# Optimization experiments

Measured on AMD Instinct MI355X. Metric: run time of the kernel, lower is better.

Reference implementation:

```python
import jax, jax.numpy as jnp
import numpy as np
import math

B, T, D, H = 4, 2048, 1024, 16
DH = D // H

def setup_inputs() -> dict:
    key = jax.random.key(0)
    k1, k2, k3, k4, k5 = jax.random.split(key, 5)
    s = 1.0 / math.sqrt(D)
    x = jax.random.normal(k1, (B, T, D), dtype=jnp.float32)
    # causal mask: 1 where attention allowed (j <= i), 0 elsewhere
    mask = jnp.tril(jnp.ones((T, T), dtype=jnp.float32))[None, None, :, :]
    W_qkv = jax.random.normal(k2, (D, 3 * D), dtype=jnp.float32) * s
    b_qkv = jax.random.normal(k3, (3 * D,), dtype=jnp.float32) * 0.02
    W_proj = jax.random.normal(k4, (D, D), dtype=jnp.float32) * s
    b_proj = jax.random.normal(k5, (D,), dtype=jnp.float32) * 0.02
    return {"x": x, "mask": mask, "W_qkv": W_qkv, "b_qkv": b_qkv,
            "W_proj": W_proj, "b_proj": b_proj}

def reference(x, mask, W_qkv, b_qkv, W_proj, b_proj):
    # qkv: [B,T,3D] -> [3,B,H,T,DH]
    qkv = x @ W_qkv + b_qkv
    qkv = qkv.reshape(B, T, 3, H, DH).transpose(2, 0, 3, 1, 4)
    q, k, v = qkv[0], qkv[1], qkv[2]
    scores = jnp.einsum('bhqd,bhkd->bhqk', q, k) / math.sqrt(DH)
    scores = jnp.where(mask == 0, -jnp.inf, scores)
    attn = jax.nn.softmax(scores, axis=-1)  # dropout p=0 -> identity
    out = jnp.einsum('bhqk,bhkd->bhqd', attn, v)
    out = out.transpose(0, 2, 1, 3).reshape(B, T, D)
    return out @ W_proj + b_proj
```

## Files before the change

kernel.cpp:

```cpp
#include <hip/hip_runtime.h>
#include <hip/hip_bf16.h>

typedef __attribute__((ext_vector_type(8))) short short8;
typedef __attribute__((ext_vector_type(4))) float f32x4;
typedef __attribute__((ext_vector_type(16))) float f32x16;
typedef __attribute__((ext_vector_type(4))) unsigned int u32x4;

#define DEV static __device__ __forceinline__

DEV unsigned short bfc(float f) {
    __bf16 h = (__bf16)f;
    return __builtin_bit_cast(unsigned short, h);
}

DEV unsigned int pack2bf(float lo, float hi) {
    return (unsigned int)bfc(lo) | ((unsigned int)bfc(hi) << 16);
}

DEV void gload16(const void* g, void* l) {
    __builtin_amdgcn_global_load_lds(
        (const __attribute__((address_space(1))) unsigned int*)g,
        (__attribute__((address_space(3))) unsigned int*)l, 16, 0, 0);
}

__global__ void cvt_bf16_kernel(const float* __restrict__ in,
                                unsigned short* __restrict__ out, int n4) {
    int stride = gridDim.x * blockDim.x;
    for (int i = blockIdx.x * blockDim.x + threadIdx.x; i < n4; i += stride) {
        float4 v = reinterpret_cast<const float4*>(in)[i];
        ushort4 o;
        o.x = bfc(v.x); o.y = bfc(v.y); o.z = bfc(v.z); o.w = bfc(v.w);
        reinterpret_cast<ushort4*>(out)[i] = o;
    }
}

__global__ void transpose_cvt_kernel(const float* __restrict__ in,
                                     unsigned short* __restrict__ out,
                                     int K, int N) {
    __shared__ float tile[32][33];
    int n0 = blockIdx.x * 32, k0 = blockIdx.y * 32;
    int tx = threadIdx.x & 31, ty = threadIdx.x >> 5;
    #pragma unroll
    for (int i = 0; i < 32; i += 8)
        tile[ty + i][tx] = in[(size_t)(k0 + ty + i) * N + n0 + tx];
    __syncthreads();
    #pragma unroll
    for (int i = 0; i < 32; i += 8)
        out[(size_t)(n0 + ty + i) * K + k0 + tx] = bfc(tile[tx][ty + i]);
}

template <int EPI>
__global__ __launch_bounds__(256) void gemm_bt(
    const unsigned short* __restrict__ A,
    const unsigned short* __restrict__ Bt,
    const float* __restrict__ bias,
    unsigned short* __restrict__ oQ,
    unsigned short* __restrict__ oK,
    unsigned short* __restrict__ oVt,
    float* __restrict__ oP,
    int M, int N, int K) {
    __shared__ unsigned short As[128 * 32];
    __shared__ unsigned short Bs[128 * 32];
    const int tid = threadIdx.x;
    const int wid = tid >> 6, lane = tid & 63;
    const int r = lane & 15, g = lane >> 4;
    const int wm = wid >> 1, wn = wid & 1;
    const int bm = blockIdx.x, bn = blockIdx.y;

    f32x4 acc[4][4];
    #pragma unroll
    for (int i = 0; i < 4; i++)
        #pragma unroll
        for (int j = 0; j < 4; j++) acc[i][j] = (f32x4)(0.f);

    const int nk = K >> 5;
    for (int kt = 0; kt < nk; ++kt) {
        const int k0 = kt << 5;
        __syncthreads();
        #pragma unroll
        for (int it = 0; it < 2; ++it) {
            int c = it * 256 + wid * 64 + lane;
            int row = c >> 2, cc = c & 3;
            int ccs = cc ^ ((row >> 1) & 3);
            gload16(A + (size_t)(bm * 128 + row) * K + k0 + ccs * 8,
                    (char*)As + (it * 256 + wid * 64) * 16);
            gload16(Bt + (size_t)(bn * 128 + row) * K + k0 + ccs * 8,
                    (char*)Bs + (it * 256 + wid * 64) * 16);
        }
        __syncthreads();
        short8 af[4], bfr[4];
        #pragma unroll
        for (int mi = 0; mi < 4; ++mi) {
            int row = wm * 64 + mi * 16 + r;
            af[mi] = *(const short8*)((const char*)As + row * 64 +
                                      ((g ^ ((row >> 1) & 3)) << 4));
        }
        #pragma unroll
        for (int ni = 0; ni < 4; ++ni) {
            int row = wn * 64 + ni * 16 + r;
            bfr[ni] = *(const short8*)((const char*)Bs + row * 64 +
                                       ((g ^ ((row >> 1) & 3)) << 4));
        }
        #pragma unroll
        for (int mi = 0; mi < 4; ++mi)
            #pragma unroll
            for (int ni = 0; ni < 4; ++ni)
                acc[mi][ni] = __builtin_amdgcn_mfma_f32_16x16x32_bf16(
                    af[mi], bfr[ni], acc[mi][ni], 0, 0, 0);
    }

    const float QSCALE = 0.18033688011112042f;
    #pragma unroll
    for (int ni = 0; ni < 4; ++ni) {
        int n = bn * 128 + wn * 64 + ni * 16 + r;
        float bb = bias[n];
        #pragma unroll
        for (int mi = 0; mi < 4; ++mi) {
            #pragma unroll
            for (int rr = 0; rr < 4; ++rr) {
                int m = bm * 128 + wm * 64 + mi * 16 + g * 4 + rr;
                float v = acc[mi][ni][rr] + bb;
                if (EPI == 0) {
                    int b = m >> 11, t = m & 2047;
                    int s = n >> 10, hh = (n >> 6) & 15, dh = n & 63;
                    size_t bh = (size_t)(b * 16 + hh);
                    if (s == 0)      oQ[(bh * 2048 + t) * 64 + dh] = bfc(v * QSCALE);
                    else if (s == 1) oK[(bh * 2048 + t) * 64 + dh] = bfc(v);
                    else             oVt[(bh * 64 + dh) * 2048 + t] = bfc(v);
                } else {
                    oP[(size_t)m * N + n] = v;
                }
            }
        }
    }
}

__global__ __launch_bounds__(512, 2) void attn_kernel(
    const unsigned short* __restrict__ Q,
    const unsigned short* __restrict__ Kb,
    const unsigned short* __restrict__ Vt,
    unsigned short* __restrict__ O) {
    __shared__ unsigned short Ks[2 * 128 * 64];
    __shared__ unsigned short Vs[2 * 64 * 128];
    const int tid = threadIdx.x, wid = tid >> 6, lane = tid & 63;
    const int ln31 = lane & 31, hi = lane >> 5;

    const int l = blockIdx.y * 8 + blockIdx.x;
    const int u = l & 255, v = l >> 8;
    const int bh = v * 32 + (u >> 3);
    const int qt = v ? (7 - (u & 7)) : (u & 7);

    const size_t hoff = (size_t)bh * 2048 * 64;
    const int qrow0 = qt * 256 + wid * 32;
    const int tq = qrow0 + ln31;
    const float NEG_INF = -__builtin_inff();

    short8 qf[4];
    #pragma unroll
    for (int st = 0; st < 4; ++st)
        qf[st] = *(const short8*)(Q + hoff + (size_t)tq * 64 + st * 16 + hi * 8);

    f32x16 oacc[2];
    oacc[0] = (f32x16)(0.f); oacc[1] = (f32x16)(0.f);
    float mrow = NEG_INF, lrow = 0.f;

    const unsigned short* Kh = Kb + hoff;
    const unsigned short* Vh = Vt + hoff;

    auto stage = [&](int buf, int kvb) {
        #pragma unroll
        for (int it = 0; it < 2; ++it) {
            int c = it * 512 + tid;
            int krow = c >> 3, kcc = c & 7;
            int kccs = kcc ^ (krow & 7);
            gload16(Kh + (size_t)(kvb + krow) * 64 + kccs * 8,
                    (char*)Ks + buf * 16384 + c * 16);
            int vrow = c >> 4, vcc = c & 15;
            int vccs = vcc ^ (vrow & 15);
            gload16(Vh + (size_t)vrow * 2048 + kvb + vccs * 8,
                    (char*)Vs + buf * 16384 + c * 16);
        }
    };

    const int nkv = 2 * qt + 2;
    stage(0, 0);
    for (int kv = 0; kv < nkv; ++kv) {
        const int kvb = kv * 128;
        const int cur = kv & 1;
        __syncthreads();
        if (kv + 1 < nkv) stage(cur ^ 1, kvb + 128);

        const char* Kbase = (const char*)Ks + cur * 16384;
        const char* Vbase = (const char*)Vs + cur * 16384;

        #pragma unroll
        for (int sub = 0; sub < 2; ++sub) {
            const int kvs = kvb + sub * 64;
            if (kvs > qrow0) continue;

            f32x16 s0 = (f32x16)(0.f), s1 = (f32x16)(0.f);
            __builtin_amdgcn_s_setprio(1);
            #pragma unroll
            for (int st = 0; st < 4; ++st) {
                int row0 = sub * 64 + ln31, row1 = sub * 64 + 32 + ln31;
                short8 kf0 = *(const short8*)(Kbase + row0 * 128 +
                                              (((2 * st + hi) ^ (row0 & 7)) << 4));
                short8 kf1 = *(const short8*)(Kbase + row1 * 128 +
                                              (((2 * st + hi) ^ (row1 & 7)) << 4));
                s0 = __builtin_amdgcn_mfma_f32_32x32x16_bf16(kf0, qf[st], s0, 0, 0, 0);
                s1 = __builtin_amdgcn_mfma_f32_32x32x16_bf16(kf1, qf[st], s1, 0, 0, 0);
            }
            __builtin_amdgcn_s_setprio(0);

            short8 vf[4][2];
            #pragma unroll
            for (int m = 0; m < 4; ++m)
                #pragma unroll
                for (int d = 0; d < 2; ++d) {
                    int row = d * 32 + ln31;
                    int slot = (sub * 8 + 2 * m + hi) ^ (row & 15);
                    vf[m][d] = *(const short8*)(Vbase + row * 256 + (slot << 4));
                }

            if (kvs + 63 > qrow0) {
                const int lim = tq - kvs;
                #pragma unroll
                for (int j = 0; j < 16; ++j) {
                    int krel = (j & 3) + 8 * (j >> 2) + 4 * hi;
                    if (krel > lim)      s0[j] = NEG_INF;
                    if (krel + 32 > lim) s1[j] = NEG_INF;
                }
            }
            float ma = fmaxf(s0[0], s0[1]), mb = fmaxf(s0[2], s0[3]);
            float mc = fmaxf(s1[0], s1[1]), md = fmaxf(s1[2], s1[3]);
            #pragma unroll
            for (int j = 4; j < 16; j += 4) {
                ma = fmaxf(ma, fmaxf(s0[j], s0[j+1]));
                mb = fmaxf(mb, fmaxf(s0[j+2], s0[j+3]));
                mc = fmaxf(mc, fmaxf(s1[j], s1[j+1]));
                md = fmaxf(md, fmaxf(s1[j+2], s1[j+3]));
            }
            float mloc = fmaxf(fmaxf(ma, mb), fmaxf(mc, md));
            mloc = fmaxf(mloc, __shfl_xor(mloc, 32));
            float mnew = fmaxf(mrow, mloc);
            if (!__all(mloc <= mrow)) {
                float alpha = exp2f(mrow - mnew);
                lrow *= alpha;
                #pragma unroll
                for (int j = 0; j < 16; ++j) { oacc[0][j] *= alpha; oacc[1][j] *= alpha; }
            }
            mrow = mnew;
            float la = 0.f, lb = 0.f, lc = 0.f, ld = 0.f;
            #pragma unroll
            for (int j = 0; j < 16; j += 2) {
                float p00 = exp2f(s0[j] - mnew), p01 = exp2f(s0[j+1] - mnew);
                float p10 = exp2f(s1[j] - mnew), p11 = exp2f(s1[j+1] - mnew);
                s0[j] = p00; s0[j+1] = p01; s1[j] = p10; s1[j+1] = p11;
                la += p00; lb += p01; lc += p10; ld += p11;
            }
            float ls = (la + lb) + (lc + ld);
            ls += __shfl_xor(ls, 32);
            lrow += ls;

            __builtin_amdgcn_s_setprio(1);
            #pragma unroll
            for (int m = 0; m < 4; ++m) {
                const int h = m & 1;
                float pa0, pa1, pb0, pb1, pc0, pc1, pd0, pd1;
                if (m < 2) {
                    pa0 = s0[8*h+0]; pa1 = s0[8*h+1]; pc0 = s0[8*h+2]; pc1 = s0[8*h+3];
                    pb0 = s0[8*h+4]; pb1 = s0[8*h+5]; pd0 = s0[8*h+6]; pd1 = s0[8*h+7];
                } else {
                    pa0 = s1[8*h+0]; pa1 = s1[8*h+1]; pc0 = s1[8*h+2]; pc1 = s1[8*h+3];
                    pb0 = s1[8*h+4]; pb1 = s1[8*h+5]; pd0 = s1[8*h+6]; pd1 = s1[8*h+7];
                }
                unsigned int pkA = pack2bf(pa0, pa1), pkC = pack2bf(pc0, pc1);
                unsigned int pkB = pack2bf(pb0, pb1), pkD = pack2bf(pd0, pd1);
                unsigned int oA = __shfl_xor(pkA, 32), oB = __shfl_xor(pkB, 32);
                unsigned int oC = __shfl_xor(pkC, 32), oD = __shfl_xor(pkD, 32);
                u32x4 w;
                w.x = hi ? oB : pkA;
                w.y = hi ? oD : pkC;
                w.z = hi ? pkB : oA;
                w.w = hi ? pkD : oC;
                short8 pfrag = __builtin_bit_cast(short8, w);
                #pragma unroll
                for (int d = 0; d < 2; ++d)
                    oacc[d] = __builtin_amdgcn_mfma_f32_32x32x16_bf16(vf[m][d], pfrag, oacc[d], 0, 0, 0);
            }
            __builtin_amdgcn_s_setprio(0);
        }
    }

    const int b = bh >> 4, h = bh & 15;
    const float rinv = 1.0f / lrow;
    unsigned short* orow = O + (size_t)(b * 2048 + tq) * 1024 + h * 64;
    #pragma unroll
    for (int d = 0; d < 2; ++d)
        #pragma unroll
        for (int u2 = 0; u2 < 4; ++u2) {
            int dh0 = d * 32 + u2 * 8 + 4 * hi;
            uint2 w;
            w.x = pack2bf(oacc[d][4*u2+0] * rinv, oacc[d][4*u2+1] * rinv);
            w.y = pack2bf(oacc[d][4*u2+2] * rinv, oacc[d][4*u2+3] * rinv);
            *(uint2*)(orow + dh0) = w;
        }
}

extern "C" void kernel_launch(void* const* d_in, const int* in_sizes, int n_in,
                              void* d_out, int out_size, void* d_ws, size_t ws_size,
                              hipStream_t stream) {
    const float* x     = (const float*)d_in[0];
    const float* Wqkv  = (const float*)d_in[2];
    const float* bqkv  = (const float*)d_in[3];
    const float* Wproj = (const float*)d_in[4];
    const float* bproj = (const float*)d_in[5];
    float* out = (float*)d_out;

    char* ws = (char*)d_ws;
    unsigned short* xb  = (unsigned short*)(ws);
    unsigned short* Ob  = (unsigned short*)(ws);
    unsigned short* WqT = (unsigned short*)(ws + (16u << 20));
    unsigned short* WpT = (unsigned short*)(ws + (22u << 20));
    unsigned short* Qb  = (unsigned short*)(ws + (24u << 20));
    unsigned short* Kb  = (unsigned short*)(ws + (40u << 20));
    unsigned short* Vt  = (unsigned short*)(ws + (56u << 20));

    cvt_bf16_kernel<<<2048, 256, 0, stream>>>(x, xb, (8192 * 1024) / 4);
    transpose_cvt_kernel<<<dim3(96, 32), 256, 0, stream>>>(Wqkv, WqT, 1024, 3072);
    transpose_cvt_kernel<<<dim3(32, 32), 256, 0, stream>>>(Wproj, WpT, 1024, 1024);
    gemm_bt<0><<<dim3(64, 24), 256, 0, stream>>>(xb, WqT, bqkv, Qb, Kb, Vt, nullptr,
                                                 8192, 3072, 1024);
    attn_kernel<<<dim3(8, 64), 512, 0, stream>>>(Qb, Kb, Vt, Ob);
    gemm_bt<1><<<dim3(64, 8), 256, 0, stream>>>(Ob, WpT, bproj, nullptr, nullptr,
                                                nullptr, out, 8192, 1024, 1024);
}
```

Measured before the change: 212.9 us.

## Split attention KV tiles across wave pairs and merge softmax partials in LDS

Each attention block now covers 128 query rows instead of 256, and the grid doubles to 1024 blocks. The 8 waves form two groups of four that each process one 64-key half of every 128-key tile, with the query tile order assigned heaviest-first. At the end the two partial softmax states (running max, row sum, output accumulator) are combined through LDS before the bf16 output is written. This raises block count and per-block parallelism for the causal workload, at the cost of an extra LDS round trip, two more barriers, and twice as many K/V tile loads per query row.

```diff
diff --git a/kernel.cpp b/kernel.cpp
--- a/kernel.cpp
+++ b/kernel.cpp
@@ -140,18 +140,21 @@
     const unsigned short* __restrict__ Kb,
     const unsigned short* __restrict__ Vt,
     unsigned short* __restrict__ O) {
-    __shared__ unsigned short Ks[2 * 128 * 64];
-    __shared__ unsigned short Vs[2 * 64 * 128];
+    __shared__ f32x4 ldsraw[4096];
+    unsigned short* Ks = (unsigned short*)ldsraw;
+    unsigned short* Vs = (unsigned short*)ldsraw + 16384;
     const int tid = threadIdx.x, wid = tid >> 6, lane = tid & 63;
     const int ln31 = lane & 31, hi = lane >> 5;
-
-    const int l = blockIdx.y * 8 + blockIdx.x;
-    const int u = l & 255, v = l >> 8;
-    const int bh = v * 32 + (u >> 3);
-    const int qt = v ? (7 - (u & 7)) : (u & 7);
+    const int rg = wid & 3, pv = wid >> 2;
+
+    const int l = blockIdx.y * 16 + blockIdx.x;
+    const int i = l & 511;
+    const int g = i >> 6;
+    const int bh = i & 63;
+    const int s = (l < 512) ? (15 - g) : (7 - g);
 
     const size_t hoff = (size_t)bh * 2048 * 64;
-    const int qrow0 = qt * 256 + wid * 32;
+    const int qrow0 = s * 128 + rg * 32;
     const int tq = qrow0 + ln31;
     const float NEG_INF = -__builtin_inff();
 
@@ -182,7 +185,7 @@
         }
     };
 
-    const int nkv = 2 * qt + 2;
+    const int nkv = s + 1;
     stage(0, 0);
     for (int kv = 0; kv < nkv; ++kv) {
         const int kvb = kv * 128;
@@ -190,19 +193,15 @@
         __syncthreads();
         if (kv + 1 < nkv) stage(cur ^ 1, kvb + 128);
 
-        const char* Kbase = (const char*)Ks + cur * 16384;
-        const char* Vbase = (const char*)Vs + cur * 16384;
-
-        #pragma unroll
-        for (int sub = 0; sub < 2; ++sub) {
-            const int kvs = kvb + sub * 64;
-            if (kvs > qrow0) continue;
-
+        const int kvs = kvb + pv * 64;
+        if (kvs <= qrow0) {
+            const char* Kbase = (const char*)Ks + cur * 16384;
+            const char* Vbase = (const char*)Vs + cur * 16384;
             f32x16 s0 = (f32x16)(0.f), s1 = (f32x16)(0.f);
             __builtin_amdgcn_s_setprio(1);
             #pragma unroll
             for (int st = 0; st < 4; ++st) {
-                int row0 = sub * 64 + ln31, row1 = sub * 64 + 32 + ln31;
+                int row0 = pv * 64 + ln31, row1 = pv * 64 + 32 + ln31;
                 short8 kf0 = *(const short8*)(Kbase + row0 * 128 +
                                               (((2 * st + hi) ^ (row0 & 7)) << 4));
                 short8 kf1 = *(const short8*)(Kbase + row1 * 128 +
@@ -218,7 +217,7 @@
                 #pragma unroll
                 for (int d = 0; d < 2; ++d) {
                     int row = d * 32 + ln31;
-                    int slot = (sub * 8 + 2 * m + hi) ^ (row & 15);
+                    int slot = (pv * 8 + 2 * m + hi) ^ (row & 15);
                     vf[m][d] = *(const short8*)(Vbase + row * 256 + (slot << 4));
                 }
 
@@ -292,19 +291,42 @@
         }
     }
 
-    const int b = bh >> 4, h = bh & 15;
-    const float rinv = 1.0f / lrow;
-    unsigned short* orow = O + (size_t)(b * 2048 + tq) * 1024 + h * 64;
-    #pragma unroll
-    for (int d = 0; d < 2; ++d)
-        #pragma unroll
-        for (int u2 = 0; u2 < 4; ++u2) {
-            int dh0 = d * 32 + u2 * 8 + 4 * hi;
-            uint2 w;
-            w.x = pack2bf(oacc[d][4*u2+0] * rinv, oacc[d][4*u2+1] * rinv);
-            w.y = pack2bf(oacc[d][4*u2+2] * rinv, oacc[d][4*u2+3] * rinv);
-            *(uint2*)(orow + dh0) = w;
-        }
+    __syncthreads();
+    float* pb = (float*)ldsraw;
+    float* base = pb + (rg * 34) * 64 + lane;
+    if (pv == 0) {
+        base[0] = mrow;
+        base[64] = lrow;
+        #pragma unroll
+        for (int j = 0; j < 16; ++j) {
+            base[(2 + j) * 64]  = oacc[0][j];
+            base[(18 + j) * 64] = oacc[1][j];
+        }
+    }
+    __syncthreads();
+    if (pv == 1) {
+        float m1 = base[0], l1 = base[64];
+        float m = fmaxf(m1, mrow);
+        float a1 = exp2f(m1 - m), a2 = exp2f(mrow - m);
+        float linv = 1.0f / (l1 * a1 + lrow * a2);
+        float c1 = a1 * linv, c2 = a2 * linv;
+        const int b = bh >> 4, h = bh & 15;
+        unsigned short* orow = O + (size_t)(b * 2048 + tq) * 1024 + h * 64;
+        #pragma unroll
+        for (int d = 0; d < 2; ++d)
+            #pragma unroll
+            for (int u2 = 0; u2 < 4; ++u2) {
+                int dh0 = d * 32 + u2 * 8 + 4 * hi;
+                float e0 = base[(2 + d * 16 + 4 * u2 + 0) * 64] * c1 + oacc[d][4*u2+0] * c2;
+                float e1 = base[(2 + d * 16 + 4 * u2 + 1) * 64] * c1 + oacc[d][4*u2+1] * c2;
+                float e2 = base[(2 + d * 16 + 4 * u2 + 2) * 64] * c1 + oacc[d][4*u2+2] * c2;
+                float e3 = base[(2 + d * 16 + 4 * u2 + 3) * 64] * c1 + oacc[d][4*u2+3] * c2;
+                uint2 w;
+                w.x = pack2bf(e0, e1);
+                w.y = pack2bf(e2, e3);
+                *(uint2*)(orow + dh0) = w;
+            }
+    }
 }
 
 extern "C" void kernel_launch(void* const* d_in, const int* in_sizes, int n_in,
@@ -331,7 +353,7 @@
     transpose_cvt_kernel<<<dim3(32, 32), 256, 0, stream>>>(Wproj, WpT, 1024, 1024);
     gemm_bt<0><<<dim3(64, 24), 256, 0, stream>>>(xb, WqT, bqkv, Qb, Kb, Vt, nullptr,
                                                  8192, 3072, 1024);
-    attn_kernel<<<dim3(8, 64), 512, 0, stream>>>(Qb, Kb, Vt, Ob);
+    attn_kernel<<<dim3(16, 64), 512, 0, stream>>>(Qb, Kb, Vt, Ob);
     gemm_bt<1><<<dim3(64, 8), 256, 0, stream>>>(Ob, WpT, bproj, nullptr, nullptr,
                                                 nullptr, out, 8192, 1024, 1024);
 }
```

After: 217.7 us. 2.2% more time.
